# Kernel tuning notes

Hardware: AMD Instinct MI355X
Metric: run time of the kernel (lower is better)

## Reference

```python
import jax, jax.numpy as jnp
import numpy as np

B, T, D_TOKEN = 32, 2048, 1024
N_HEADS, D_HEAD = 16, 64


def setup_inputs() -> dict:
    key = jax.random.key(0)
    k1, k2, k3, k4 = jax.random.split(key, 4)
    scale = 1.0 / np.sqrt(D_TOKEN)
    return {
        "x": jax.random.normal(k1, (B, T, D_TOKEN), dtype=jnp.float32),
        # torch Linear weight layout: [out_features, in_features]
        "W_heads": jax.random.normal(k2, (N_HEADS, D_HEAD, D_TOKEN), dtype=jnp.float32) * scale,
        "W_proj": jax.random.normal(k3, (D_TOKEN, N_HEADS * D_HEAD), dtype=jnp.float32) * scale,
        "b_proj": jax.random.normal(k4, (D_TOKEN,), dtype=jnp.float32) * scale,
    }


def reference(x, W_heads, W_proj, b_proj):
    b, t, d = x.shape
    n, h, _ = W_heads.shape
    # per-head bias-free linear projections; concat along channel == reshape of stacked einsum
    heads = jnp.einsum('btd,nhd->btnh', x, W_heads).reshape(b, t, n * h)  # [b, t, N*d_head]
    # sum-pool over tokens ('b t c -> b c', 'sum')
    x_concat = heads.sum(axis=1)  # [b, N*d_head]
    # output projection (with bias)
    return x_concat @ W_proj.T + b_proj  # [b, d_token]
```

## Files before the change

### kernel.cpp

```cpp
#include <hip/hip_runtime.h>

#define B 32
#define T 2048
#define D 1024

constexpr int TCHUNK = 64;
constexpr int NTC    = T / TCHUNK;

__global__ __launch_bounds__(256) void reduce_tokens_partial(const float* __restrict__ x,
                                                             float* __restrict__ p) {
    const int blk = blockIdx.x;
    const int b   = blk >> 5;
    const int tc  = blk & (NTC - 1);
    const int d4  = threadIdx.x * 4;

    const float* base = x + ((size_t)b * T + (size_t)tc * TCHUNK) * D + d4;

    float4 acc = make_float4(0.f, 0.f, 0.f, 0.f);
    #pragma unroll 8
    for (int t = 0; t < TCHUNK; ++t) {
        float4 v = *(const float4*)(base + (size_t)t * D);
        acc.x += v.x; acc.y += v.y; acc.z += v.z; acc.w += v.w;
    }

    *(float4*)(p + ((size_t)b * NTC + tc) * D + d4) = acc;
}

__global__ __launch_bounds__(256) void reduce_partials(const float* __restrict__ p,
                                                       float* __restrict__ s) {
    const int b = blockIdx.x >> 2;
    const int d = (blockIdx.x & 3) * 256 + threadIdx.x;

    const float* pp = p + (size_t)b * NTC * D + d;
    float acc = 0.f;
    #pragma unroll
    for (int tc = 0; tc < NTC; ++tc)
        acc += pp[(size_t)tc * D];
    s[(size_t)b * D + d] = acc;
}

__global__ __launch_bounds__(256) void gemv_b4(const float* __restrict__ A,
                                               const float* __restrict__ W,
                                               const float* __restrict__ bias,
                                               float* __restrict__ out,
                                               int has_bias) {
    const int g    = blockIdx.x * 4 + (threadIdx.x >> 6);
    const int lane = threadIdx.x & 63;
    const int b0   = (g & 7) * 4;
    const int c    = g >> 3;

    const float* w  = W + (size_t)c * D;
    const float* a0 = A + (size_t)b0 * D;

    float acc0 = 0.f, acc1 = 0.f, acc2 = 0.f, acc3 = 0.f;
    #pragma unroll
    for (int k = 0; k < 4; ++k) {
        const int d = k * 256 + lane * 4;
        float4 wv = *(const float4*)(w + d);
        float4 a;
        a = *(const float4*)(a0 + d);
        acc0 += a.x * wv.x + a.y * wv.y + a.z * wv.z + a.w * wv.w;
        a = *(const float4*)(a0 + D + d);
        acc1 += a.x * wv.x + a.y * wv.y + a.z * wv.z + a.w * wv.w;
        a = *(const float4*)(a0 + 2 * D + d);
        acc2 += a.x * wv.x + a.y * wv.y + a.z * wv.z + a.w * wv.w;
        a = *(const float4*)(a0 + 3 * D + d);
        acc3 += a.x * wv.x + a.y * wv.y + a.z * wv.z + a.w * wv.w;
    }

    #pragma unroll
    for (int off = 32; off > 0; off >>= 1) {
        acc0 += __shfl_xor(acc0, off, 64);
        acc1 += __shfl_xor(acc1, off, 64);
        acc2 += __shfl_xor(acc2, off, 64);
        acc3 += __shfl_xor(acc3, off, 64);
    }

    if (lane == 0) {
        const float bb = has_bias ? bias[c] : 0.f;
        out[(size_t)(b0 + 0) * D + c] = acc0 + bb;
        out[(size_t)(b0 + 1) * D + c] = acc1 + bb;
        out[(size_t)(b0 + 2) * D + c] = acc2 + bb;
        out[(size_t)(b0 + 3) * D + c] = acc3 + bb;
    }
}

extern "C" void kernel_launch(void* const* d_in, const int* in_sizes, int n_in,
                              void* d_out, int out_size, void* d_ws, size_t ws_size,
                              hipStream_t stream) {
    const float* x  = (const float*)d_in[0];
    const float* Wh = (const float*)d_in[1];
    const float* Wp = (const float*)d_in[2];
    const float* bp = (const float*)d_in[3];
    float* out = (float*)d_out;

    float* p   = (float*)d_ws;
    float* s   = p + (size_t)B * NTC * D;
    float* tmp = s + (size_t)B * D;

    reduce_tokens_partial<<<B * NTC, 256, 0, stream>>>(x, p);
    reduce_partials<<<128, 256, 0, stream>>>(p, s);
    gemv_b4<<<(B / 4) * D / 4, 256, 0, stream>>>(s,   Wh, nullptr, tmp, 0);
    gemv_b4<<<(B / 4) * D / 4, 256, 0, stream>>>(tmp, Wp, bp,      out, 1);
}
```

Baseline: 380.4 us.

## Stage batch rows in LDS for 8-batch GEMV and vectorize partial reduction

```diff
diff --git a/kernel.cpp b/kernel.cpp
--- a/kernel.cpp
+++ b/kernel.cpp
@@ -16,72 +16,79 @@
 
     const float* base = x + ((size_t)b * T + (size_t)tc * TCHUNK) * D + d4;
 
-    float4 acc = make_float4(0.f, 0.f, 0.f, 0.f);
-    #pragma unroll 8
-    for (int t = 0; t < TCHUNK; ++t) {
-        float4 v = *(const float4*)(base + (size_t)t * D);
-        acc.x += v.x; acc.y += v.y; acc.z += v.z; acc.w += v.w;
+    float4 acc0 = make_float4(0.f, 0.f, 0.f, 0.f);
+    float4 acc1 = make_float4(0.f, 0.f, 0.f, 0.f);
+    #pragma unroll 4
+    for (int t = 0; t < TCHUNK; t += 2) {
+        float4 v0 = *(const float4*)(base + (size_t)t * D);
+        float4 v1 = *(const float4*)(base + (size_t)(t + 1) * D);
+        acc0.x += v0.x; acc0.y += v0.y; acc0.z += v0.z; acc0.w += v0.w;
+        acc1.x += v1.x; acc1.y += v1.y; acc1.z += v1.z; acc1.w += v1.w;
     }
+    acc0.x += acc1.x; acc0.y += acc1.y; acc0.z += acc1.z; acc0.w += acc1.w;
 
-    *(float4*)(p + ((size_t)b * NTC + tc) * D + d4) = acc;
+    *(float4*)(p + ((size_t)b * NTC + tc) * D + d4) = acc0;
 }
 
 __global__ __launch_bounds__(256) void reduce_partials(const float* __restrict__ p,
                                                        float* __restrict__ s) {
-    const int b = blockIdx.x >> 2;
-    const int d = (blockIdx.x & 3) * 256 + threadIdx.x;
+    const int col = blockIdx.x * 256 + threadIdx.x;
+    const int b   = col >> 8;
+    const int d4  = (col & 255) * 4;
 
-    const float* pp = p + (size_t)b * NTC * D + d;
-    float acc = 0.f;
-    #pragma unroll
-    for (int tc = 0; tc < NTC; ++tc)
-        acc += pp[(size_t)tc * D];
-    s[(size_t)b * D + d] = acc;
+    const float* pp = p + (size_t)b * NTC * D + d4;
+    float4 acc = make_float4(0.f, 0.f, 0.f, 0.f);
+    #pragma unroll 8
+    for (int tc = 0; tc < NTC; ++tc) {
+        float4 v = *(const float4*)(pp + (size_t)tc * D);
+        acc.x += v.x; acc.y += v.y; acc.z += v.z; acc.w += v.w;
+    }
+    *(float4*)(s + (size_t)b * D + d4) = acc;
 }
 
-__global__ __launch_bounds__(256) void gemv_b4(const float* __restrict__ A,
+__global__ __launch_bounds__(256) void gemv_b8(const float* __restrict__ A,
                                                const float* __restrict__ W,
                                                const float* __restrict__ bias,
                                                float* __restrict__ out,
                                                int has_bias) {
-    const int g    = blockIdx.x * 4 + (threadIdx.x >> 6);
+    __shared__ float4 lds[2048];
+
+    const int bg   = blockIdx.x & 3;
+    const int c    = (blockIdx.x >> 2) * 4 + (threadIdx.x >> 6);
     const int lane = threadIdx.x & 63;
-    const int b0   = (g & 7) * 4;
-    const int c    = g >> 3;
+    const int b0   = bg * 8;
 
-    const float* w  = W + (size_t)c * D;
-    const float* a0 = A + (size_t)b0 * D;
+    const float4* a4 = (const float4*)(A + (size_t)b0 * D);
+    #pragma unroll
+    for (int k = 0; k < 8; ++k)
+        lds[k * 256 + threadIdx.x] = a4[k * 256 + threadIdx.x];
+    __syncthreads();
 
-    float acc0 = 0.f, acc1 = 0.f, acc2 = 0.f, acc3 = 0.f;
+    const float4* w4 = (const float4*)(W + (size_t)c * D);
+
+    float acc[8] = {0.f, 0.f, 0.f, 0.f, 0.f, 0.f, 0.f, 0.f};
     #pragma unroll
     for (int k = 0; k < 4; ++k) {
-        const int d = k * 256 + lane * 4;
-        float4 wv = *(const float4*)(w + d);
-        float4 a;
-        a = *(const float4*)(a0 + d);
-        acc0 += a.x * wv.x + a.y * wv.y + a.z * wv.z + a.w * wv.w;
-        a = *(const float4*)(a0 + D + d);
-        acc1 += a.x * wv.x + a.y * wv.y + a.z * wv.z + a.w * wv.w;
-        a = *(const float4*)(a0 + 2 * D + d);
-        acc2 += a.x * wv.x + a.y * wv.y + a.z * wv.z + a.w * wv.w;
-        a = *(const float4*)(a0 + 3 * D + d);
-        acc3 += a.x * wv.x + a.y * wv.y + a.z * wv.z + a.w * wv.w;
+        float4 wv = w4[k * 64 + lane];
+        #pragma unroll
+        for (int j = 0; j < 8; ++j) {
+            float4 av = lds[j * 256 + k * 64 + lane];
+            acc[j] += av.x * wv.x + av.y * wv.y + av.z * wv.z + av.w * wv.w;
+        }
     }
 
     #pragma unroll
     for (int off = 32; off > 0; off >>= 1) {
-        acc0 += __shfl_xor(acc0, off, 64);
-        acc1 += __shfl_xor(acc1, off, 64);
-        acc2 += __shfl_xor(acc2, off, 64);
-        acc3 += __shfl_xor(acc3, off, 64);
+        #pragma unroll
+        for (int j = 0; j < 8; ++j)
+            acc[j] += __shfl_xor(acc[j], off, 64);
     }
 
     if (lane == 0) {
         const float bb = has_bias ? bias[c] : 0.f;
-        out[(size_t)(b0 + 0) * D + c] = acc0 + bb;
-        out[(size_t)(b0 + 1) * D + c] = acc1 + bb;
-        out[(size_t)(b0 + 2) * D + c] = acc2 + bb;
-        out[(size_t)(b0 + 3) * D + c] = acc3 + bb;
+        #pragma unroll
+        for (int j = 0; j < 8; ++j)
+            out[(size_t)(b0 + j) * D + c] = acc[j] + bb;
     }
 }
 
@@ -99,7 +106,7 @@
     float* tmp = s + (size_t)B * D;
 
     reduce_tokens_partial<<<B * NTC, 256, 0, stream>>>(x, p);
-    reduce_partials<<<128, 256, 0, stream>>>(p, s);
-    gemv_b4<<<(B / 4) * D / 4, 256, 0, stream>>>(s,   Wh, nullptr, tmp, 0);
-    gemv_b4<<<(B / 4) * D / 4, 256, 0, stream>>>(tmp, Wp, bp,      out, 1);
+    reduce_partials<<<32, 256, 0, stream>>>(p, s);
+    gemv_b8<<<1024, 256, 0, stream>>>(s,   Wh, nullptr, tmp, 0);
+    gemv_b8<<<1024, 256, 0, stream>>>(tmp, Wp, bp,      out, 1);
 }
```

Measured after the change: 380.9 us. No clear change (+0.1%).
